# Performance work log

Measured on AMD Instinct MI355X. Metric: run time of the kernel, lower is better.

## Reference

```python
import jax, jax.numpy as jnp
import numpy as np


def setup_inputs() -> dict:
    key = jax.random.key(0)
    ks = jax.random.split(key, 5)
    B, S, H = 64, 1024, 1024
    scale = 1.0 / np.sqrt(H)
    return {
        "decoder_hidden": jax.random.normal(ks[0], (B, H), jnp.float32),
        "encoder_outputs": jax.random.normal(ks[1], (B, S, H), jnp.float32),
        "W1": jax.random.normal(ks[2], (H, H), jnp.float32) * scale,
        "W2": jax.random.normal(ks[3], (H, H), jnp.float32) * scale,
        "v": jax.random.normal(ks[4], (H,), jnp.float32) * scale,
    }


def reference(decoder_hidden, encoder_outputs, W1, W2, v):
    # W1 @ decoder_hidden: [B, H] computed once, broadcast over src_len
    dh_proj = jnp.einsum("bh,oh->bo", decoder_hidden, W1)          # [B, H]
    enc_proj = jnp.einsum("bsh,oh->bso", encoder_outputs, W2)      # [B, S, H]
    energy = jnp.tanh(dh_proj[:, None, :] + enc_proj)              # [B, S, H]
    scores = jnp.einsum("bsh,h->bs", energy, v)                    # [B, S]
    attention_weights = jax.nn.softmax(scores, axis=-1)            # [B, S]
    context = jnp.einsum("bs,bsh->bh", attention_weights, encoder_outputs)
    return (context, attention_weights)
```

## Files before the change

### kernel.cpp

```cpp
#include <hip/hip_runtime.h>
#include <hip/hip_bf16.h>
#include <cmath>

#define Hdim 1024
#define Bdim 64
#define Sdim 1024

typedef __attribute__((ext_vector_type(4))) float f32x4;
typedef __attribute__((ext_vector_type(8))) short s16x8;
typedef __attribute__((ext_vector_type(4))) unsigned int u32x4;

static __device__ __forceinline__ unsigned short f2bf(float f) {
  unsigned int u = __builtin_bit_cast(unsigned int, f);
  unsigned int r = (u + 0x7fffu + ((u >> 16) & 1u)) >> 16;
  return (unsigned short)r;
}

static __device__ __forceinline__ float bf2f(unsigned short u) {
  return __builtin_bit_cast(float, (unsigned int)u << 16);
}

#define TANH_C 2.885390081777927f


static __device__ __forceinline__ void stage_rows64(const float* __restrict__ src,
                                                    unsigned short* As, int tid) {
  #pragma unroll 4
  for (int i = 0; i < 32; ++i) {
    int c = tid + i * 256;
    int row = c >> 7;
    int k8 = (c & 127) << 3;
    const float4* p = reinterpret_cast<const float4*>(src + row * Hdim + k8);
    float4 a = p[0];
    float4 b = p[1];
    union { unsigned short us[8]; u32x4 v; } pk;
    pk.us[0] = f2bf(a.x); pk.us[1] = f2bf(a.y); pk.us[2] = f2bf(a.z); pk.us[3] = f2bf(a.w);
    pk.us[4] = f2bf(b.x); pk.us[5] = f2bf(b.y); pk.us[6] = f2bf(b.z); pk.us[7] = f2bf(b.w);
    int idx = row * Hdim + (k8 ^ ((row & 7) << 3));
    *reinterpret_cast<u32x4*>(&As[idx]) = pk.v;
  }
}

static __device__ __forceinline__ s16x8 lda_full(const unsigned short* As, int row, int k) {
  int idx = row * Hdim + (k ^ ((row & 7) << 3));
  return *reinterpret_cast<const s16x8*>(&As[idx]);
}

static __device__ __forceinline__ s16x8 ldb_g(const unsigned short* __restrict__ Wb,
                                              const float* __restrict__ Wf,
                                              int use_bf, int o, int k) {
  if (use_bf) {
    return *reinterpret_cast<const s16x8*>(&Wb[o * Hdim + k]);
  } else {
    const float4* p = reinterpret_cast<const float4*>(Wf + o * Hdim + k);
    float4 a = p[0];
    float4 b = p[1];
    union { unsigned short us[8]; s16x8 v; } pk;
    pk.us[0] = f2bf(a.x); pk.us[1] = f2bf(a.y); pk.us[2] = f2bf(a.z); pk.us[3] = f2bf(a.w);
    pk.us[4] = f2bf(b.x); pk.us[5] = f2bf(b.y); pk.us[6] = f2bf(b.z); pk.us[7] = f2bf(b.w);
    return pk.v;
  }
}

__global__ void cast_bf16_kernel(const float* __restrict__ src,
                                 unsigned short* __restrict__ dst) {
  int i = blockIdx.x * 256 + threadIdx.x;
  const f32x4* p = reinterpret_cast<const f32x4*>(src) + i * 2;
  f32x4 a = __builtin_nontemporal_load(p);
  f32x4 b = __builtin_nontemporal_load(p + 1);
  union { unsigned short us[8]; u32x4 v; } pk;
  pk.us[0] = f2bf(a[0]); pk.us[1] = f2bf(a[1]); pk.us[2] = f2bf(a[2]); pk.us[3] = f2bf(a[3]);
  pk.us[4] = f2bf(b[0]); pk.us[5] = f2bf(b[1]); pk.us[6] = f2bf(b[2]); pk.us[7] = f2bf(b[3]);
  *reinterpret_cast<u32x4*>(dst + i * 8) = pk.v;
}

__global__ __launch_bounds__(256, 1) void proj_kernel(
    const float* __restrict__ dh, const float* __restrict__ W1f,
    const unsigned short* __restrict__ W1b, float* __restrict__ out, int use_bf) {
  __shared__ unsigned short As[64 * Hdim];
  int tid = threadIdx.x;
  stage_rows64(dh, As, tid);
  __syncthreads();
  int w = tid >> 6, lane = tid & 63;
  int lo = lane & 15, hi = lane >> 4;
  int o = blockIdx.x * 16 + lo;
  f32x4 acc = {0.f, 0.f, 0.f, 0.f};
  for (int k0 = 0; k0 < Hdim; k0 += 32) {
    int k = k0 + hi * 8;
    s16x8 bfrag = ldb_g(W1b, W1f, use_bf, o, k);
    s16x8 afrag = lda_full(As, w * 16 + lo, k);
    acc = __builtin_amdgcn_mfma_f32_16x16x32_bf16(afrag, bfrag, acc, 0, 0, 0);
  }
  #pragma unroll
  for (int r = 0; r < 4; ++r)
    out[(w * 16 + hi * 4 + r) * Hdim + o] = acc[r];
}

#define SBM 256
#define SBN 256
#define SBK 64

__global__ __launch_bounds__(512, 1) void score_mfma_kernel(
    const unsigned short* __restrict__ encb,
    const unsigned short* __restrict__ W2b,
    const float* __restrict__ dhp, const float* __restrict__ v,
    float* __restrict__ scores) {
  __shared__ unsigned short As[2][SBM * SBK];
  __shared__ unsigned short Bs[2][SBN * SBK];
  int tid = threadIdx.x;
  int bid = blockIdx.x;
  int swz = (bid & 7) * 128 + (bid >> 3);
  int mp = swz >> 2;
  int np = swz & 3;
  int row0 = mp * SBM;
  int b = row0 >> 10;
  int w = tid >> 6, lane = tid & 63;
  int wr = w >> 2, wc = w & 3;
  int lo = lane & 15, hi = lane >> 4;
  int xorv = (lo & 7) << 4;

  int srow = tid >> 3;
  int gc = (tid & 7) ^ (srow & 7);
  const unsigned short* gA0 = encb + (size_t)(row0 + srow) * Hdim + gc * 8;
  const unsigned short* gB0 = W2b + (size_t)(np * SBN + srow) * Hdim + gc * 8;

  auto SA = [&](int g, int t, int s) {
    __builtin_amdgcn_global_load_lds(
        (const __attribute__((address_space(1))) unsigned int*)(gA0 + (size_t)g * 64 * Hdim + t * SBK),
        (__attribute__((address_space(3))) unsigned int*)(&As[s][(g * 512 + w * 64) * 8]), 16, 0, 0);
  };
  auto SB = [&](int g, int t, int s) {
    __builtin_amdgcn_global_load_lds(
        (const __attribute__((address_space(1))) unsigned int*)(gB0 + (size_t)g * 64 * Hdim + t * SBK),
        (__attribute__((address_space(3))) unsigned int*)(&Bs[s][(g * 512 + w * 64) * 8]), 16, 0, 0);
  };

  f32x4 acc[2][2][4][2] = {};
  s16x8 af[2][4][2];
  s16x8 bf[2][2];

  SA(0, 0, 0); SB(0, 0, 0);
  SA(1, 0, 0); SB(1, 0, 0);
  SA(2, 0, 0); SA(3, 0, 0);
  SB(2, 0, 0); SB(3, 0, 0);
  asm volatile("s_waitcnt vmcnt(4)" ::: "memory");
  __builtin_amdgcn_s_barrier();
  asm volatile("" ::: "memory");

  for (int it = 0; it < 8; ++it) {
    int t1 = 2 * it + 1;
    int t2 = (it < 7) ? 2 * it + 2 : 15;
    #pragma unroll
    for (int p = 0; p < 8; ++p) {
      const int grp = p >> 2;
      const int q = p & 3;
      const int mh = (q == 0 || q == 3) ? 0 : 1;
      const int nh = q >> 1;
      const int rs = grp;
      const int ss = grp ^ 1;
      const int st = grp ? t2 : t1;

      if (q == 0)      { SA(0, st, ss); SB(0, st, ss); }
      else if (q == 1) { SA(1, st, ss); SB(1, st, ss); }
      else if (q == 2) { SA(2, st, ss); SA(3, st, ss); }
      else             { SB(2, st, ss); SB(3, st, ss); }

      const char* Ab = (const char*)As[rs];
      const char* Bb = (const char*)Bs[rs];
      if (q == 0 || q == 1) {
        #pragma unroll
        for (int m = 0; m < 4; ++m)
          #pragma unroll
          for (int ks = 0; ks < 2; ++ks)
            af[mh][m][ks] = *reinterpret_cast<const s16x8*>(
                Ab + (mh * 128 + wr * 64 + m * 16 + lo) * 128 + ((ks * 64 + hi * 16) ^ xorv));
      }
      if (q == 0 || q == 2) {
        #pragma unroll
        for (int n = 0; n < 2; ++n)
          #pragma unroll
          for (int ks = 0; ks < 2; ++ks)
            bf[n][ks] = *reinterpret_cast<const s16x8*>(
                Bb + (nh * 128 + wc * 32 + n * 16 + lo) * 128 + ((ks * 64 + hi * 16) ^ xorv));
      }

      asm volatile("s_waitcnt vmcnt(4)" ::: "memory");
      __builtin_amdgcn_s_barrier();
      asm volatile("" ::: "memory");

      __builtin_amdgcn_s_setprio(1);
      #pragma unroll
      for (int ks = 0; ks < 2; ++ks)
        #pragma unroll
        for (int m = 0; m < 4; ++m)
          #pragma unroll
          for (int n = 0; n < 2; ++n)
            acc[mh][nh][m][n] = __builtin_amdgcn_mfma_f32_16x16x32_bf16(
                af[mh][m][ks], bf[n][ks], acc[mh][nh][m][n], 0, 0, 0);
      __builtin_amdgcn_s_setprio(0);
    }
  }

  float psum[2][4][4] = {};
  #pragma unroll
  for (int nh = 0; nh < 2; ++nh)
    #pragma unroll
    for (int n = 0; n < 2; ++n) {
      int o = np * SBN + nh * 128 + wc * 32 + n * 16 + lo;
      float dv = dhp[b * Hdim + o];
      float vv = v[o];
      float vv2 = 2.f * vv;
      #pragma unroll
      for (int mh = 0; mh < 2; ++mh)
        #pragma unroll
        for (int m = 0; m < 4; ++m)
          #pragma unroll
          for (int r = 0; r < 4; ++r) {
            float x = acc[mh][nh][m][n][r] + dv;
            float e2 = __builtin_amdgcn_exp2f(x * TANH_C);
            float rc = __builtin_amdgcn_rcpf(1.f + e2);
            psum[mh][m][r] += vv - vv2 * rc;
          }
    }
  #pragma unroll
  for (int mask = 1; mask < 16; mask <<= 1)
    #pragma unroll
    for (int mh = 0; mh < 2; ++mh)
      #pragma unroll
      for (int m = 0; m < 4; ++m)
        #pragma unroll
        for (int r = 0; r < 4; ++r)
          psum[mh][m][r] += __shfl_xor(psum[mh][m][r], mask, 64);
  if (lo == 0) {
    #pragma unroll
    for (int mh = 0; mh < 2; ++mh)
      #pragma unroll
      for (int m = 0; m < 4; ++m)
        #pragma unroll
        for (int r = 0; r < 4; ++r)
          atomicAdd(&scores[row0 + mh * 128 + wr * 64 + m * 16 + hi * 4 + r], psum[mh][m][r]);
  }
}

#define BKt 64

__global__ __launch_bounds__(256, 3) void score_kernel(
    const float* __restrict__ enc, const float* __restrict__ W2f,
    const unsigned short* __restrict__ W2b, const float* __restrict__ dhp,
    const float* __restrict__ v, float* __restrict__ scores, int use_bf) {
  __shared__ unsigned short As[64 * BKt];
  int tid = threadIdx.x;
  int bid = blockIdx.x;
  int f = (bid & 7) * 512 + (bid >> 3);
  int rg = f >> 2;
  int oc = f & 3;
  int row0 = rg * 64;
  int b = row0 >> 10;
  int w = tid >> 6, lane = tid & 63;
  int lo = lane & 15, hi = lane >> 4;
  int n0 = oc * 256 + w * 64;

  const unsigned short* pB[4];
  const float* pBf[4];
  #pragma unroll
  for (int n = 0; n < 4; ++n) {
    int o = n0 + n * 16 + lo;
    pB[n]  = W2b + (size_t)o * Hdim + hi * 8;
    pBf[n] = W2f + (size_t)o * Hdim + hi * 8;
  }

  f32x4 acc[4][4] = {};

  for (int t = 0; t < 16; ++t) {
    int k0 = t * BKt;
    __syncthreads();
    #pragma unroll
    for (int cc = 0; cc < 2; ++cc) {
      int c = tid + cc * 256;
      int row = c >> 3;
      int j = c & 7;
      const float4* p = reinterpret_cast<const float4*>(
          enc + (size_t)(row0 + row) * Hdim + k0 + j * 8);
      float4 a = p[0];
      float4 bb = p[1];
      union { unsigned short us[8]; u32x4 v4; } pk;
      pk.us[0] = f2bf(a.x);  pk.us[1] = f2bf(a.y);  pk.us[2] = f2bf(a.z);  pk.us[3] = f2bf(a.w);
      pk.us[4] = f2bf(bb.x); pk.us[5] = f2bf(bb.y); pk.us[6] = f2bf(bb.z); pk.us[7] = f2bf(bb.w);
      int idx = row * BKt + ((j * 8) ^ ((row & 7) << 3));
      *reinterpret_cast<u32x4*>(&As[idx]) = pk.v4;
    }
    __syncthreads();

    #pragma unroll
    for (int ks = 0; ks < 2; ++ks) {
      s16x8 bfrag[4];
      #pragma unroll
      for (int n = 0; n < 4; ++n) {
        if (use_bf) {
          bfrag[n] = *reinterpret_cast<const s16x8*>(pB[n] + ks * 32);
        } else {
          const float4* p = reinterpret_cast<const float4*>(pBf[n] + ks * 32);
          float4 a = p[0];
          float4 bb = p[1];
          union { unsigned short us[8]; s16x8 v4; } pk;
          pk.us[0] = f2bf(a.x);  pk.us[1] = f2bf(a.y);  pk.us[2] = f2bf(a.z);  pk.us[3] = f2bf(a.w);
          pk.us[4] = f2bf(bb.x); pk.us[5] = f2bf(bb.y); pk.us[6] = f2bf(bb.z); pk.us[7] = f2bf(bb.w);
          bfrag[n] = pk.v4;
        }
      }
      #pragma unroll
      for (int m = 0; m < 4; ++m) {
        int kk = ks * 32 + hi * 8;
        s16x8 afrag = *reinterpret_cast<const s16x8*>(
            &As[(m * 16 + lo) * BKt + (kk ^ ((lo & 7) << 3))]);
        #pragma unroll
        for (int n = 0; n < 4; ++n)
          acc[m][n] = __builtin_amdgcn_mfma_f32_16x16x32_bf16(afrag, bfrag[n], acc[m][n], 0, 0, 0);
      }
    }
    #pragma unroll
    for (int n = 0; n < 4; ++n) { pB[n] += BKt; pBf[n] += BKt; }
  }

  float psum[4][4] = {};
  #pragma unroll
  for (int n = 0; n < 4; ++n) {
    int o = n0 + n * 16 + lo;
    float dv = dhp[b * Hdim + o];
    float vv = v[o];
    float vv2 = 2.f * vv;
    #pragma unroll
    for (int m = 0; m < 4; ++m)
      #pragma unroll
      for (int r = 0; r < 4; ++r) {
        float x = acc[m][n][r] + dv;
        float e2 = __builtin_amdgcn_exp2f(x * TANH_C);
        float rc = __builtin_amdgcn_rcpf(1.f + e2);
        psum[m][r] += vv - vv2 * rc;
      }
  }
  #pragma unroll
  for (int mask = 1; mask < 16; mask <<= 1)
    #pragma unroll
    for (int m = 0; m < 4; ++m)
      #pragma unroll
      for (int r = 0; r < 4; ++r)
        psum[m][r] += __shfl_xor(psum[m][r], mask, 64);
  if (lo == 0) {
    #pragma unroll
    for (int m = 0; m < 4; ++m)
      #pragma unroll
      for (int r = 0; r < 4; ++r)
        atomicAdd(&scores[row0 + m * 16 + hi * 4 + r], psum[m][r]);
  }
}

__global__ __launch_bounds__(256, 1) void softmax_kernel(float* __restrict__ attn) {
  __shared__ float redm[4];
  __shared__ float reds[4];
  int b = blockIdx.x, tid = threadIdx.x;
  float4 x = *reinterpret_cast<float4*>(attn + b * Sdim + tid * 4);
  float m = fmaxf(fmaxf(x.x, x.y), fmaxf(x.z, x.w));
  #pragma unroll
  for (int mask = 1; mask < 64; mask <<= 1) m = fmaxf(m, __shfl_xor(m, mask, 64));
  if ((tid & 63) == 0) redm[tid >> 6] = m;
  __syncthreads();
  m = fmaxf(fmaxf(redm[0], redm[1]), fmaxf(redm[2], redm[3]));
  float4 e;
  e.x = expf(x.x - m); e.y = expf(x.y - m); e.z = expf(x.z - m); e.w = expf(x.w - m);
  float s = e.x + e.y + e.z + e.w;
  #pragma unroll
  for (int mask = 1; mask < 64; mask <<= 1) s += __shfl_xor(s, mask, 64);
  if ((tid & 63) == 0) reds[tid >> 6] = s;
  __syncthreads();
  s = reds[0] + reds[1] + reds[2] + reds[3];
  float inv = 1.f / s;
  e.x *= inv; e.y *= inv; e.z *= inv; e.w *= inv;
  *reinterpret_cast<float4*>(attn + b * Sdim + tid * 4) = e;
}

__global__ __launch_bounds__(256, 1) void context_bf_kernel(
    const unsigned short* __restrict__ encb, const float* __restrict__ attn,
    float* __restrict__ ctx) {
  int b = blockIdx.x >> 4;
  int chunk = blockIdx.x & 15;
  int tid = threadIdx.x;
  int h0 = tid * 4;
  const unsigned short* ebase = encb + ((size_t)(b * Sdim + chunk * 64)) * Hdim + h0;
  const float* abase = attn + b * Sdim + chunk * 64;
  float4 acc = {0.f, 0.f, 0.f, 0.f};
  #pragma unroll 4
  for (int s = 0; s < 64; ++s) {
    float wgt = abase[s];
    ushort4 ev = *reinterpret_cast<const ushort4*>(ebase + (size_t)s * Hdim);
    acc.x += wgt * bf2f(ev.x);
    acc.y += wgt * bf2f(ev.y);
    acc.z += wgt * bf2f(ev.z);
    acc.w += wgt * bf2f(ev.w);
  }
  float* c = ctx + b * Hdim + h0;
  atomicAdd(c + 0, acc.x);
  atomicAdd(c + 1, acc.y);
  atomicAdd(c + 2, acc.z);
  atomicAdd(c + 3, acc.w);
}

__global__ __launch_bounds__(256, 1) void context_kernel(
    const float* __restrict__ enc, const float* __restrict__ attn,
    float* __restrict__ ctx) {
  int b = blockIdx.x >> 3;
  int chunk = blockIdx.x & 7;
  int tid = threadIdx.x;
  int h0 = tid * 4;
  const float* ebase = enc + ((size_t)(b * Sdim + chunk * 128)) * Hdim + h0;
  const float* abase = attn + b * Sdim + chunk * 128;
  float4 acc = {0.f, 0.f, 0.f, 0.f};
  #pragma unroll 4
  for (int s = 0; s < 128; ++s) {
    float wgt = abase[s];
    float4 ev = *reinterpret_cast<const float4*>(ebase + (size_t)s * Hdim);
    acc.x += wgt * ev.x; acc.y += wgt * ev.y; acc.z += wgt * ev.z; acc.w += wgt * ev.w;
  }
  float* c = ctx + b * Hdim + h0;
  atomicAdd(c + 0, acc.x);
  atomicAdd(c + 1, acc.y);
  atomicAdd(c + 2, acc.z);
  atomicAdd(c + 3, acc.w);
}

extern "C" void kernel_launch(void* const* d_in, const int* in_sizes, int n_in,
                              void* d_out, int out_size, void* d_ws, size_t ws_size,
                              hipStream_t stream) {
  const float* dh  = (const float*)d_in[0];
  const float* enc = (const float*)d_in[1];
  const float* W1  = (const float*)d_in[2];
  const float* W2  = (const float*)d_in[3];
  const float* v   = (const float*)d_in[4];
  float* out_ctx  = (float*)d_out;
  float* out_attn = out_ctx + Bdim * Hdim;

  int use_bf = (ws_size >= 4ull * 1024 * 1024) ? 1 : 0;
  int big_ws = (ws_size >= 133ull * 1024 * 1024) ? 1 : 0;
  unsigned short* W1b  = (unsigned short*)d_ws;
  unsigned short* W2b  = W1b + 1024 * 1024;
  unsigned short* encb = W2b + 1024 * 1024;

  if (use_bf) {
    cast_bf16_kernel<<<512, 256, 0, stream>>>(W1, W1b);
    cast_bf16_kernel<<<512, 256, 0, stream>>>(W2, W2b);
  }
  if (big_ws) {
    cast_bf16_kernel<<<32768, 256, 0, stream>>>(enc, encb);
  }

  proj_kernel<<<64, 256, 0, stream>>>(dh, W1, W1b, out_ctx, use_bf);

  hipMemsetAsync(out_attn, 0, (size_t)Bdim * Sdim * sizeof(float), stream);
  if (big_ws) {
    score_mfma_kernel<<<1024, 512, 0, stream>>>(encb, W2b, out_ctx, v, out_attn);
  } else {
    score_kernel<<<4096, 256, 0, stream>>>(enc, W2, W2b, out_ctx, v, out_attn, use_bf);
  }

  softmax_kernel<<<Bdim, 256, 0, stream>>>(out_attn);

  hipMemsetAsync(out_ctx, 0, (size_t)Bdim * Hdim * sizeof(float), stream);
  if (big_ws) {
    context_bf_kernel<<<1024, 256, 0, stream>>>(encb, out_attn, out_ctx);
  } else {
    context_kernel<<<512, 256, 0, stream>>>(enc, out_attn, out_ctx);
  }
}
```

Before: 290.0 us.

## Prefetch MFMA LDS fragments after compute and relax score kernel launch bounds

Moves the LDS fragment reads in the score GEMM to after each MFMA phase, double-buffering the B fragments by n-half. The next sub-tile's operands are read while the current compute drains, and the next stage's first fragments are read at the end of each group. Global-to-LDS stage issue is regrouped, and the wait/barrier now sits after compute with a vmcnt(2) threshold instead of vmcnt(4). Launch bounds change to request 2 blocks per CU. That tightens the register budget for a kernel holding 128 accumulator floats per thread and risks spills, while the 128 KB LDS footprint likely prevents a second block from fitting anyway.

```diff
diff --git a/kernel.cpp b/kernel.cpp
--- a/kernel.cpp
+++ b/kernel.cpp
@@ -100,7 +100,7 @@
 #define SBN 256
 #define SBK 64
 
-__global__ __launch_bounds__(512, 1) void score_mfma_kernel(
+__global__ __launch_bounds__(512, 2) void score_mfma_kernel(
     const unsigned short* __restrict__ encb,
     const unsigned short* __restrict__ W2b,
     const float* __restrict__ dhp, const float* __restrict__ v,
@@ -137,15 +137,32 @@
 
   f32x4 acc[2][2][4][2] = {};
   s16x8 af[2][4][2];
-  s16x8 bf[2][2];
-
-  SA(0, 0, 0); SB(0, 0, 0);
-  SA(1, 0, 0); SB(1, 0, 0);
-  SA(2, 0, 0); SA(3, 0, 0);
-  SB(2, 0, 0); SB(3, 0, 0);
-  asm volatile("s_waitcnt vmcnt(4)" ::: "memory");
+  s16x8 bf[2][2][2];
+
+  auto LD_AF = [&](int mh_, const char* Ab) {
+    #pragma unroll
+    for (int m = 0; m < 4; ++m)
+      #pragma unroll
+      for (int ks = 0; ks < 2; ++ks)
+        af[mh_][m][ks] = *reinterpret_cast<const s16x8*>(
+            Ab + (mh_ * 128 + wr * 64 + m * 16 + lo) * 128 + ((ks * 64 + hi * 16) ^ xorv));
+  };
+  auto LD_BF = [&](int nh_, const char* Bb) {
+    #pragma unroll
+    for (int n = 0; n < 2; ++n)
+      #pragma unroll
+      for (int ks = 0; ks < 2; ++ks)
+        bf[nh_][n][ks] = *reinterpret_cast<const s16x8*>(
+            Bb + (nh_ * 128 + wc * 32 + n * 16 + lo) * 128 + ((ks * 64 + hi * 16) ^ xorv));
+  };
+
+  SA(0, 0, 0); SA(1, 0, 0); SB(0, 0, 0); SB(1, 0, 0);
+  SA(2, 0, 0); SA(3, 0, 0); SB(2, 0, 0); SB(3, 0, 0);
+  asm volatile("s_waitcnt vmcnt(0)" ::: "memory");
   __builtin_amdgcn_s_barrier();
   asm volatile("" ::: "memory");
+  LD_AF(0, (const char*)As[0]);
+  LD_BF(0, (const char*)Bs[0]);
 
   for (int it = 0; it < 8; ++it) {
     int t1 = 2 * it + 1;
@@ -154,39 +171,16 @@
     for (int p = 0; p < 8; ++p) {
       const int grp = p >> 2;
       const int q = p & 3;
-      const int mh = (q == 0 || q == 3) ? 0 : 1;
-      const int nh = q >> 1;
       const int rs = grp;
       const int ss = grp ^ 1;
       const int st = grp ? t2 : t1;
-
-      if (q == 0)      { SA(0, st, ss); SB(0, st, ss); }
-      else if (q == 1) { SA(1, st, ss); SB(1, st, ss); }
+      const int mh = (q == 1 || q == 2) ? 1 : 0;
+      const int nh = q >> 1;
+
+      if (q == 0)      { SA(0, st, ss); SA(1, st, ss); }
+      else if (q == 1) { SB(0, st, ss); SB(1, st, ss); }
       else if (q == 2) { SA(2, st, ss); SA(3, st, ss); }
       else             { SB(2, st, ss); SB(3, st, ss); }
-
-      const char* Ab = (const char*)As[rs];
-      const char* Bb = (const char*)Bs[rs];
-      if (q == 0 || q == 1) {
-        #pragma unroll
-        for (int m = 0; m < 4; ++m)
-          #pragma unroll
-          for (int ks = 0; ks < 2; ++ks)
-            af[mh][m][ks] = *reinterpret_cast<const s16x8*>(
-                Ab + (mh * 128 + wr * 64 + m * 16 + lo) * 128 + ((ks * 64 + hi * 16) ^ xorv));
-      }
-      if (q == 0 || q == 2) {
-        #pragma unroll
-        for (int n = 0; n < 2; ++n)
-          #pragma unroll
-          for (int ks = 0; ks < 2; ++ks)
-            bf[n][ks] = *reinterpret_cast<const s16x8*>(
-                Bb + (nh * 128 + wc * 32 + n * 16 + lo) * 128 + ((ks * 64 + hi * 16) ^ xorv));
-      }
-
-      asm volatile("s_waitcnt vmcnt(4)" ::: "memory");
-      __builtin_amdgcn_s_barrier();
-      asm volatile("" ::: "memory");
 
       __builtin_amdgcn_s_setprio(1);
       #pragma unroll
@@ -196,8 +190,21 @@
           #pragma unroll
           for (int n = 0; n < 2; ++n)
             acc[mh][nh][m][n] = __builtin_amdgcn_mfma_f32_16x16x32_bf16(
-                af[mh][m][ks], bf[n][ks], acc[mh][nh][m][n], 0, 0, 0);
+                af[mh][m][ks], bf[nh][n][ks], acc[mh][nh][m][n], 0, 0, 0);
       __builtin_amdgcn_s_setprio(0);
+
+      if (q == 0) {
+        LD_AF(1, (const char*)As[rs]);
+      } else if (q == 1) {
+        LD_BF(1, (const char*)Bs[rs]);
+      } else if (q == 3) {
+        LD_AF(0, (const char*)As[ss]);
+        LD_BF(0, (const char*)Bs[ss]);
+      }
+
+      asm volatile("s_waitcnt vmcnt(2)" ::: "memory");
+      __builtin_amdgcn_s_barrier();
+      asm volatile("" ::: "memory");
     }
   }
 
```

Result: no change. 294.1 us (+1.4%).
